# Kernel tuning notes

Measured on AMD Instinct MI355X. Metric: run time of the kernel, lower is better.

Reference implementation:

```python
import jax, jax.numpy as jnp
import numpy as np

B, IN, OUT = 8192, 4096, 4096

def setup_inputs() -> dict:
    key = jax.random.key(0)
    ks = jax.random.split(key, 7)
    # sigma params initialized near -3 as in the torch module
    return {
        "x": jax.random.normal(ks[0], (B, IN), dtype=jnp.float32),
        "weight_mu": 0.1 * jax.random.normal(ks[1], (OUT, IN), dtype=jnp.float32),
        "weight_sigma": -3.0 + 0.1 * jax.random.normal(ks[2], (OUT, IN), dtype=jnp.float32),
        "bias_mu": 0.1 * jax.random.normal(ks[3], (OUT,), dtype=jnp.float32),
        "bias_sigma": -3.0 + 0.1 * jax.random.normal(ks[4], (OUT,), dtype=jnp.float32),
        "eps_w": jax.random.normal(ks[5], (OUT, IN), dtype=jnp.float32),
        "eps_b": jax.random.normal(ks[6], (OUT,), dtype=jnp.float32),
    }

def reference(x, weight_mu, weight_sigma, bias_mu, bias_sigma, eps_w, eps_b):
    # Reparameterized sample: w = mu + exp(sigma) * eps
    weight = weight_mu + jnp.exp(weight_sigma) * eps_w          # [OUT, IN]
    bias = bias_mu + jnp.exp(bias_sigma) * eps_b                # [OUT]
    out = jnp.einsum('bi,oi->bo', x, weight) + bias             # [B, OUT]
    # KL(q || N(0,1)); note log(var) == 2*sigma
    weight_var = jnp.exp(2.0 * weight_sigma)
    bias_var = jnp.exp(2.0 * bias_sigma)
    kl_w = -0.5 * jnp.sum(1.0 + 2.0 * weight_sigma - weight_mu ** 2 - weight_var)
    kl_b = -0.5 * jnp.sum(1.0 + 2.0 * bias_sigma - bias_mu ** 2 - bias_var)
    return out, kl_w + kl_b
```

## Files before the change

### kernel.cpp

```cpp
#include <hip/hip_runtime.h>

#define MDIM 8192
#define NDIM 4096
#define KDIM 4096
#define BK 32

typedef unsigned short u16;
typedef __attribute__((ext_vector_type(8))) short short8;
typedef __attribute__((ext_vector_type(4))) float f32x4;

__device__ __forceinline__ u16 f2b(float f) {
  unsigned u = __float_as_uint(f);
  u += 0x7FFFu + ((u >> 16) & 1u);
  return (u16)(u >> 16);
}
__device__ __forceinline__ unsigned pk2(float a, float b) {
  return (unsigned)f2b(a) | ((unsigned)f2b(b) << 16);
}

__device__ __forceinline__ void async16(const u16* g, u16* l) {
  __builtin_amdgcn_global_load_lds(
      (const __attribute__((address_space(1))) unsigned*)g,
      (__attribute__((address_space(3))) unsigned*)l, 16, 0, 0);
}

__global__ __launch_bounds__(256) void k_prep_x(const float4* __restrict__ x,
                                                uint4* __restrict__ xb) {
  const int i = blockIdx.x * 256 + threadIdx.x;
  float4 a = x[2 * i], b = x[2 * i + 1];
  uint4 o;
  o.x = pk2(a.x, a.y); o.y = pk2(a.z, a.w);
  o.z = pk2(b.x, b.y); o.w = pk2(b.z, b.w);
  xb[i] = o;
}

__global__ __launch_bounds__(256) void k_prep_w(const float4* __restrict__ mu,
                                                const float4* __restrict__ sg,
                                                const float4* __restrict__ ep,
                                                uint4* __restrict__ wb,
                                                float* __restrict__ partials) {
  const int i = blockIdx.x * 256 + threadIdx.x;
  float part = 0.f;
  uint4 o;
  {
    float4 m = mu[2 * i], s = sg[2 * i], e = ep[2 * i];
    float e0 = __expf(s.x), e1 = __expf(s.y), e2 = __expf(s.z), e3 = __expf(s.w);
    o.x = pk2(m.x + e0 * e.x, m.y + e1 * e.y);
    o.y = pk2(m.z + e2 * e.z, m.w + e3 * e.w);
    part += (1.f + 2.f * s.x - m.x * m.x - e0 * e0)
          + (1.f + 2.f * s.y - m.y * m.y - e1 * e1)
          + (1.f + 2.f * s.z - m.z * m.z - e2 * e2)
          + (1.f + 2.f * s.w - m.w * m.w - e3 * e3);
  }
  {
    float4 m = mu[2 * i + 1], s = sg[2 * i + 1], e = ep[2 * i + 1];
    float e0 = __expf(s.x), e1 = __expf(s.y), e2 = __expf(s.z), e3 = __expf(s.w);
    o.z = pk2(m.x + e0 * e.x, m.y + e1 * e.y);
    o.w = pk2(m.z + e2 * e.z, m.w + e3 * e.w);
    part += (1.f + 2.f * s.x - m.x * m.x - e0 * e0)
          + (1.f + 2.f * s.y - m.y * m.y - e1 * e1)
          + (1.f + 2.f * s.z - m.z * m.z - e2 * e2)
          + (1.f + 2.f * s.w - m.w * m.w - e3 * e3);
  }
  wb[i] = o;
  for (int off = 32; off; off >>= 1) part += __shfl_down(part, off, 64);
  __shared__ float red[4];
  const int lane = threadIdx.x & 63, wv = threadIdx.x >> 6;
  if (lane == 0) red[wv] = part;
  __syncthreads();
  if (threadIdx.x == 0)
    partials[blockIdx.x] = red[0] + red[1] + red[2] + red[3];
}

__global__ __launch_bounds__(256) void k_bias(const float* __restrict__ bmu,
                                              const float* __restrict__ bsg,
                                              const float* __restrict__ bep,
                                              float* __restrict__ bias,
                                              const float* __restrict__ partials,
                                              int nPart,
                                              float* __restrict__ klOut) {
  float part = 0.f;
  for (int i = threadIdx.x; i < NDIM; i += 256) {
    float s = bsg[i], m = bmu[i];
    float es = __expf(s);
    bias[i] = m + es * bep[i];
    part += 1.f + 2.f * s - m * m - es * es;
  }
  for (int i = threadIdx.x; i < nPart; i += 256) part += partials[i];
  for (int off = 32; off; off >>= 1) part += __shfl_down(part, off, 64);
  __shared__ float red[4];
  const int lane = threadIdx.x & 63, wv = threadIdx.x >> 6;
  if (lane == 0) red[wv] = part;
  __syncthreads();
  if (threadIdx.x == 0) *klOut = -0.5f * (red[0] + red[1] + red[2] + red[3]);
}

__global__ __launch_bounds__(256) void k_gemm(const u16* __restrict__ A,
                                              const u16* __restrict__ B,
                                              const float* __restrict__ bias,
                                              float* __restrict__ C) {
  __shared__ u16 sA[128 * BK];
  __shared__ u16 sB[128 * BK];
  const int t = threadIdx.x;
  const int wave = t >> 6, lane = t & 63;
  const int bm = blockIdx.x * 128;
  const int bn = blockIdx.y * 128;
  const int wm = (wave >> 1) * 64;
  const int wn = (wave & 1) * 64;

  const int srow = lane >> 2;
  const int scol = (lane & 3) * 8;
  const u16* gA0 = A + (size_t)(bm + wave * 32 + srow) * KDIM + scol;
  const u16* gA1 = gA0 + (size_t)16 * KDIM;
  const u16* gB0 = B + (size_t)(bn + wave * 32 + srow) * KDIM + scol;
  const u16* gB1 = gB0 + (size_t)16 * KDIM;
  u16* lA0 = &sA[(wave * 32) * BK];
  u16* lA1 = &sA[(wave * 32 + 16) * BK];
  u16* lB0 = &sB[(wave * 32) * BK];
  u16* lB1 = &sB[(wave * 32 + 16) * BK];

  const int fr = lane & 15;
  const int fg = lane >> 4;

  f32x4 acc[4][4] = {};

  for (int k0 = 0; k0 < KDIM; k0 += BK) {
    async16(gA0 + k0, lA0);
    async16(gA1 + k0, lA1);
    async16(gB0 + k0, lB0);
    async16(gB1 + k0, lB1);
    __syncthreads();

    short8 af[4], bf[4];
#pragma unroll
    for (int i = 0; i < 4; ++i) {
      af[i] = *(const short8*)&sA[(wm + i * 16 + fr) * BK + fg * 8];
      bf[i] = *(const short8*)&sB[(wn + i * 16 + fr) * BK + fg * 8];
    }
#pragma unroll
    for (int i = 0; i < 4; ++i)
#pragma unroll
      for (int j = 0; j < 4; ++j)
        acc[i][j] = __builtin_amdgcn_mfma_f32_16x16x32_bf16(af[i], bf[j],
                                                            acc[i][j], 0, 0, 0);
    __syncthreads();
  }

#pragma unroll
  for (int j = 0; j < 4; ++j) {
    const int gn = bn + wn + j * 16 + fr;
    const float bv = bias[gn];
#pragma unroll
    for (int i = 0; i < 4; ++i) {
      const int gm0 = bm + wm + i * 16 + fg * 4;
      float* Cp = C + (size_t)gm0 * NDIM + gn;
#pragma unroll
      for (int r = 0; r < 4; ++r)
        Cp[(size_t)r * NDIM] = acc[i][j][r] + bv;
    }
  }
}

extern "C" void kernel_launch(void* const* d_in, const int* in_sizes, int n_in,
                              void* d_out, int out_size, void* d_ws, size_t ws_size,
                              hipStream_t stream) {
  const float* x    = (const float*)d_in[0];
  const float* wmu  = (const float*)d_in[1];
  const float* wsig = (const float*)d_in[2];
  const float* bmu  = (const float*)d_in[3];
  const float* bsig = (const float*)d_in[4];
  const float* ew   = (const float*)d_in[5];
  const float* eb   = (const float*)d_in[6];
  float* out = (float*)d_out;

  char* ws = (char*)d_ws;
  u16*   xb       = (u16*)ws;
  u16*   wb       = (u16*)(ws + 67108864);
  float* bias     = (float*)(ws + 100663296);
  float* partials = (float*)(ws + 100679680);

  k_prep_w<<<8192, 256, 0, stream>>>((const float4*)wmu, (const float4*)wsig,
                                     (const float4*)ew, (uint4*)wb, partials);
  k_prep_x<<<16384, 256, 0, stream>>>((const float4*)x, (uint4*)xb);
  k_bias<<<1, 256, 0, stream>>>(bmu, bsig, eb, bias, partials, 8192,
                                out + (size_t)MDIM * NDIM);
  dim3 grid(MDIM / 128, NDIM / 128);
  k_gemm<<<grid, 256, 0, stream>>>(xb, wb, bias, out);
}
```

Measured before the change: 705.2 us.

## Merge prep kernels, widen bias reduction, and swizzle GEMM tiles into groups

The separate weight and x bf16-conversion kernels become one launch, with blocks past 8192 converting two chunks of x each. The single-block bias/KL reduction kernel moves to 1024 threads. The GEMM grid becomes a 1D launch whose tiles are remapped into 16x16 groups so that concurrent blocks share A and B tiles in L2. The aim is fewer launches and better cache reuse in the GEMM, which dominates run time.

```diff
diff --git a/kernel.cpp b/kernel.cpp
--- a/kernel.cpp
+++ b/kernel.cpp
@@ -24,75 +24,86 @@
       (__attribute__((address_space(3))) unsigned*)l, 16, 0, 0);
 }
 
-__global__ __launch_bounds__(256) void k_prep_x(const float4* __restrict__ x,
-                                                uint4* __restrict__ xb) {
-  const int i = blockIdx.x * 256 + threadIdx.x;
-  float4 a = x[2 * i], b = x[2 * i + 1];
-  uint4 o;
-  o.x = pk2(a.x, a.y); o.y = pk2(a.z, a.w);
-  o.z = pk2(b.x, b.y); o.w = pk2(b.z, b.w);
-  xb[i] = o;
-}
-
-__global__ __launch_bounds__(256) void k_prep_w(const float4* __restrict__ mu,
-                                                const float4* __restrict__ sg,
-                                                const float4* __restrict__ ep,
-                                                uint4* __restrict__ wb,
-                                                float* __restrict__ partials) {
-  const int i = blockIdx.x * 256 + threadIdx.x;
+__global__ __launch_bounds__(256) void k_prep(const float4* __restrict__ wmu,
+                                              const float4* __restrict__ wsg,
+                                              const float4* __restrict__ wep,
+                                              uint4* __restrict__ wb,
+                                              const float4* __restrict__ x,
+                                              uint4* __restrict__ xb,
+                                              float* __restrict__ partials) {
+  const int bx = blockIdx.x;
+  if (bx < 8192) {
+    const int i = bx * 256 + (int)threadIdx.x;
+    float part = 0.f;
+    uint4 o;
+    {
+      float4 m = wmu[2 * i], s = wsg[2 * i], e = wep[2 * i];
+      float e0 = __expf(s.x), e1 = __expf(s.y), e2 = __expf(s.z), e3 = __expf(s.w);
+      o.x = pk2(m.x + e0 * e.x, m.y + e1 * e.y);
+      o.y = pk2(m.z + e2 * e.z, m.w + e3 * e.w);
+      part += (1.f + 2.f * s.x - m.x * m.x - e0 * e0)
+            + (1.f + 2.f * s.y - m.y * m.y - e1 * e1)
+            + (1.f + 2.f * s.z - m.z * m.z - e2 * e2)
+            + (1.f + 2.f * s.w - m.w * m.w - e3 * e3);
+    }
+    {
+      float4 m = wmu[2 * i + 1], s = wsg[2 * i + 1], e = wep[2 * i + 1];
+      float e0 = __expf(s.x), e1 = __expf(s.y), e2 = __expf(s.z), e3 = __expf(s.w);
+      o.z = pk2(m.x + e0 * e.x, m.y + e1 * e.y);
+      o.w = pk2(m.z + e2 * e.z, m.w + e3 * e.w);
+      part += (1.f + 2.f * s.x - m.x * m.x - e0 * e0)
+            + (1.f + 2.f * s.y - m.y * m.y - e1 * e1)
+            + (1.f + 2.f * s.z - m.z * m.z - e2 * e2)
+            + (1.f + 2.f * s.w - m.w * m.w - e3 * e3);
+    }
+    wb[i] = o;
+    for (int off = 32; off; off >>= 1) part += __shfl_down(part, off, 64);
+    __shared__ float red[4];
+    const int lane = threadIdx.x & 63, wv = threadIdx.x >> 6;
+    if (lane == 0) red[wv] = part;
+    __syncthreads();
+    if (threadIdx.x == 0)
+      partials[bx] = red[0] + red[1] + red[2] + red[3];
+  } else {
+    const int i0 = (bx - 8192) * 256 + (int)threadIdx.x;
+#pragma unroll
+    for (int c = 0; c < 2; ++c) {
+      const int i = i0 + c * (8192 * 256);
+      float4 a = x[2 * i], b = x[2 * i + 1];
+      uint4 o;
+      o.x = pk2(a.x, a.y); o.y = pk2(a.z, a.w);
+      o.z = pk2(b.x, b.y); o.w = pk2(b.z, b.w);
+      xb[i] = o;
+    }
+  }
+}
+
+__global__ __launch_bounds__(1024) void k_bias(const float* __restrict__ bmu,
+                                               const float* __restrict__ bsg,
+                                               const float* __restrict__ bep,
+                                               float* __restrict__ bias,
+                                               const float* __restrict__ partials,
+                                               int nPart,
+                                               float* __restrict__ klOut) {
   float part = 0.f;
-  uint4 o;
-  {
-    float4 m = mu[2 * i], s = sg[2 * i], e = ep[2 * i];
-    float e0 = __expf(s.x), e1 = __expf(s.y), e2 = __expf(s.z), e3 = __expf(s.w);
-    o.x = pk2(m.x + e0 * e.x, m.y + e1 * e.y);
-    o.y = pk2(m.z + e2 * e.z, m.w + e3 * e.w);
-    part += (1.f + 2.f * s.x - m.x * m.x - e0 * e0)
-          + (1.f + 2.f * s.y - m.y * m.y - e1 * e1)
-          + (1.f + 2.f * s.z - m.z * m.z - e2 * e2)
-          + (1.f + 2.f * s.w - m.w * m.w - e3 * e3);
-  }
-  {
-    float4 m = mu[2 * i + 1], s = sg[2 * i + 1], e = ep[2 * i + 1];
-    float e0 = __expf(s.x), e1 = __expf(s.y), e2 = __expf(s.z), e3 = __expf(s.w);
-    o.z = pk2(m.x + e0 * e.x, m.y + e1 * e.y);
-    o.w = pk2(m.z + e2 * e.z, m.w + e3 * e.w);
-    part += (1.f + 2.f * s.x - m.x * m.x - e0 * e0)
-          + (1.f + 2.f * s.y - m.y * m.y - e1 * e1)
-          + (1.f + 2.f * s.z - m.z * m.z - e2 * e2)
-          + (1.f + 2.f * s.w - m.w * m.w - e3 * e3);
-  }
-  wb[i] = o;
-  for (int off = 32; off; off >>= 1) part += __shfl_down(part, off, 64);
-  __shared__ float red[4];
-  const int lane = threadIdx.x & 63, wv = threadIdx.x >> 6;
-  if (lane == 0) red[wv] = part;
-  __syncthreads();
-  if (threadIdx.x == 0)
-    partials[blockIdx.x] = red[0] + red[1] + red[2] + red[3];
-}
-
-__global__ __launch_bounds__(256) void k_bias(const float* __restrict__ bmu,
-                                              const float* __restrict__ bsg,
-                                              const float* __restrict__ bep,
-                                              float* __restrict__ bias,
-                                              const float* __restrict__ partials,
-                                              int nPart,
-                                              float* __restrict__ klOut) {
-  float part = 0.f;
-  for (int i = threadIdx.x; i < NDIM; i += 256) {
+  for (int i = threadIdx.x; i < NDIM; i += 1024) {
     float s = bsg[i], m = bmu[i];
     float es = __expf(s);
     bias[i] = m + es * bep[i];
     part += 1.f + 2.f * s - m * m - es * es;
   }
-  for (int i = threadIdx.x; i < nPart; i += 256) part += partials[i];
+  for (int i = threadIdx.x; i < nPart; i += 1024) part += partials[i];
   for (int off = 32; off; off >>= 1) part += __shfl_down(part, off, 64);
-  __shared__ float red[4];
+  __shared__ float red[16];
   const int lane = threadIdx.x & 63, wv = threadIdx.x >> 6;
   if (lane == 0) red[wv] = part;
   __syncthreads();
-  if (threadIdx.x == 0) *klOut = -0.5f * (red[0] + red[1] + red[2] + red[3]);
+  if (threadIdx.x == 0) {
+    float s = 0.f;
+#pragma unroll
+    for (int w = 0; w < 16; ++w) s += red[w];
+    *klOut = -0.5f * s;
+  }
 }
 
 __global__ __launch_bounds__(256) void k_gemm(const u16* __restrict__ A,
@@ -103,8 +114,14 @@
   __shared__ u16 sB[128 * BK];
   const int t = threadIdx.x;
   const int wave = t >> 6, lane = t & 63;
-  const int bm = blockIdx.x * 128;
-  const int bn = blockIdx.y * 128;
+
+  const int lin = blockIdx.x;
+  const int tile = lin >> 8, within = lin & 255;
+  const int tm = within & 15, tn = within >> 4;
+  const int sm = tile & 3, sn = tile >> 2;
+  const int bm = (sm * 16 + tm) * 128;
+  const int bn = (sn * 16 + tn) * 128;
+
   const int wm = (wave >> 1) * 64;
   const int wn = (wave & 1) * 64;
 
@@ -179,11 +196,10 @@
   float* bias     = (float*)(ws + 100663296);
   float* partials = (float*)(ws + 100679680);
 
-  k_prep_w<<<8192, 256, 0, stream>>>((const float4*)wmu, (const float4*)wsig,
-                                     (const float4*)ew, (uint4*)wb, partials);
-  k_prep_x<<<16384, 256, 0, stream>>>((const float4*)x, (uint4*)xb);
-  k_bias<<<1, 256, 0, stream>>>(bmu, bsig, eb, bias, partials, 8192,
-                                out + (size_t)MDIM * NDIM);
-  dim3 grid(MDIM / 128, NDIM / 128);
-  k_gemm<<<grid, 256, 0, stream>>>(xb, wb, bias, out);
-}
+  k_prep<<<16384, 256, 0, stream>>>((const float4*)wmu, (const float4*)wsig,
+                                    (const float4*)ew, (uint4*)wb,
+                                    (const float4*)x, (uint4*)xb, partials);
+  k_bias<<<1, 1024, 0, stream>>>(bmu, bsig, eb, bias, partials, 8192,
+                                 out + (size_t)MDIM * NDIM);
+  k_gemm<<<2048, 256, 0, stream>>>(xb, wb, bias, out);
+}
```

Result: faster. 671.8 us (-4.7%).
